# Kernel optimization log

Measured on AMD Instinct MI355X. Metric: run time of the kernel, lower is better.

The kernel has to match this reference:

```python
import jax, jax.numpy as jnp
import numpy as np

K = 64  # key_features
V = 64  # value_features


def setup_inputs() -> dict:
    key = jax.random.key(0)
    ks = jax.random.split(key, 7)
    B, IN, M = 512, 512, 2048
    H = 2 * K + V  # 192, hidden_state dim == output dim of layer
    return {
        "x": jax.random.normal(ks[0], (B, IN), dtype=jnp.float32),
        "hidden_state": jax.random.normal(ks[1], (B, H), dtype=jnp.float32),
        "content": jax.random.normal(ks[2], (B, V), dtype=jnp.float32),
        "key_mem": jax.random.normal(ks[3], (B, K, M), dtype=jnp.float32),
        "value_mem": jax.random.normal(ks[4], (B, V, M), dtype=jnp.float32),
        "W": jax.random.normal(ks[5], (H, IN + 2 * K + 2 * V), dtype=jnp.float32) * 0.02,
        "b": jax.random.normal(ks[6], (H,), dtype=jnp.float32) * 0.02,
    }


def reference(x, hidden_state, content, key_mem, value_mem, W, b):
    # dropout in eval mode (identity); relu on hidden_state
    inp = jnp.concatenate([x, jax.nn.relu(hidden_state), content], axis=1)  # [B, IN+2K+2V]
    o = inp @ W.T + b  # [B, 2K+V]
    query = o[:, :K]            # [B, K]
    # buffer.read: attention over memory slots
    scores = jnp.einsum("bkm,bk->bm", key_mem, query)   # [B, M]
    attn = jax.nn.softmax(scores, axis=1)               # [B, M]
    content_new = jnp.einsum("bvm,bm->bv", value_mem, attn)  # [B, V]
    # buffer.write (state update, returned for completeness of math; original
    # mutates buffer in place; key @ II is exactly a right-shift by one slot):
    new_key = o[:, K:2 * K]
    new_value = o[:, 2 * K:2 * K + V]
    key_mem_next = jnp.concatenate([new_key[:, :, None], key_mem[:, :, :-1]], axis=2)
    value_mem_next = jnp.concatenate([new_value[:, :, None], value_mem[:, :, :-1]], axis=2)
    del key_mem_next, value_mem_next  # forward output matches original: (o, content)
    return (o, content_new)
```

## Files before the change

kernel.cpp:

```cpp
#include <hip/hip_runtime.h>

#define KDIM 64
#define VDIM 64
#define MDIM 2048
#define BDIM 512
#define INDIM 512
#define HDIM 192
#define CIN 768
#define O_SIZE (BDIM*HDIM)

__global__ __launch_bounds__(512, 4)
void memlinear_kernel(const float* __restrict__ x,
                      const float* __restrict__ hidden,
                      const float* __restrict__ content,
                      const float* __restrict__ key_mem,
                      const float* __restrict__ value_mem,
                      const float* __restrict__ W,
                      const float* __restrict__ bias,
                      float* __restrict__ out)
{
    const int b    = blockIdx.x;
    const int tid  = threadIdx.x;
    const int lane = tid & 63;
    const int wid  = tid >> 6;

    __shared__ __align__(16) float inp[CIN];
    __shared__ float q[KDIM];
    __shared__ float red[8];
    __shared__ __align__(16) float attn_lds[MDIM];

    if (tid < INDIM) inp[tid] = x[(size_t)b*INDIM + tid];
    if (tid < HDIM)  inp[INDIM + tid] = fmaxf(hidden[(size_t)b*HDIM + tid], 0.f);
    if (tid < VDIM)  inp[INDIM + HDIM + tid] = content[(size_t)b*VDIM + tid];
    __syncthreads();

    if (tid < HDIM) {
        const float4* w4 = reinterpret_cast<const float4*>(W) + (size_t)tid * (CIN/4);
        const float4* i4 = reinterpret_cast<const float4*>(inp);
        float ax = 0.f, ay = 0.f, az = 0.f, aw = 0.f;
        #pragma unroll 8
        for (int i = 0; i < CIN/4; ++i) {
            float4 w = w4[i];
            float4 v = i4[i];
            ax = fmaf(w.x, v.x, ax);
            ay = fmaf(w.y, v.y, ay);
            az = fmaf(w.z, v.z, az);
            aw = fmaf(w.w, v.w, aw);
        }
        float o = (ax + ay) + (az + aw) + bias[tid];
        out[(size_t)b*HDIM + tid] = o;
        if (tid < KDIM) q[tid] = o;
    }
    __syncthreads();

    const float4* km4 = reinterpret_cast<const float4*>(key_mem + (size_t)b*KDIM*MDIM);
    float4 s = make_float4(0.f, 0.f, 0.f, 0.f);
    #pragma unroll 8
    for (int k = 0; k < KDIM; ++k) {
        float qk = q[k];
        float4 kk = km4[(size_t)k*(MDIM/4) + tid];
        s.x = fmaf(qk, kk.x, s.x);
        s.y = fmaf(qk, kk.y, s.y);
        s.z = fmaf(qk, kk.z, s.z);
        s.w = fmaf(qk, kk.w, s.w);
    }

    float mx = fmaxf(fmaxf(s.x, s.y), fmaxf(s.z, s.w));
    #pragma unroll
    for (int off = 32; off >= 1; off >>= 1)
        mx = fmaxf(mx, __shfl_xor(mx, off));
    if (lane == 0) red[wid] = mx;
    __syncthreads();
    float m_all = red[0];
    #pragma unroll
    for (int w = 1; w < 8; ++w) m_all = fmaxf(m_all, red[w]);

    float4 e;
    e.x = __expf(s.x - m_all);
    e.y = __expf(s.y - m_all);
    e.z = __expf(s.z - m_all);
    e.w = __expf(s.w - m_all);
    float sum = (e.x + e.y) + (e.z + e.w);
    #pragma unroll
    for (int off = 32; off >= 1; off >>= 1)
        sum += __shfl_xor(sum, off);
    __syncthreads();
    if (lane == 0) red[wid] = sum;
    __syncthreads();
    float total = 0.f;
    #pragma unroll
    for (int w = 0; w < 8; ++w) total += red[w];
    float inv = 1.0f / total;

    reinterpret_cast<float4*>(attn_lds)[tid] =
        make_float4(e.x*inv, e.y*inv, e.z*inv, e.w*inv);
    __syncthreads();

    const float4* vm4 = reinterpret_cast<const float4*>(value_mem + (size_t)b*VDIM*MDIM);
    const float4* a4  = reinterpret_cast<const float4*>(attn_lds);
    #pragma unroll
    for (int vi = 0; vi < 8; ++vi) {
        int v = wid*8 + vi;
        float px = 0.f, py = 0.f, pz = 0.f, pw = 0.f;
        #pragma unroll
        for (int i = 0; i < 8; ++i) {
            float4 vv = vm4[(size_t)v*(MDIM/4) + i*64 + lane];
            float4 aa = a4[i*64 + lane];
            px = fmaf(vv.x, aa.x, px);
            py = fmaf(vv.y, aa.y, py);
            pz = fmaf(vv.z, aa.z, pz);
            pw = fmaf(vv.w, aa.w, pw);
        }
        float p = (px + py) + (pz + pw);
        #pragma unroll
        for (int off = 32; off >= 1; off >>= 1)
            p += __shfl_xor(p, off);
        if (lane == 0) out[O_SIZE + (size_t)b*VDIM + v] = p;
    }
}

extern "C" void kernel_launch(void* const* d_in, const int* in_sizes, int n_in,
                              void* d_out, int out_size, void* d_ws, size_t ws_size,
                              hipStream_t stream) {
    const float* x         = (const float*)d_in[0];
    const float* hidden    = (const float*)d_in[1];
    const float* content   = (const float*)d_in[2];
    const float* key_mem   = (const float*)d_in[3];
    const float* value_mem = (const float*)d_in[4];
    const float* W         = (const float*)d_in[5];
    const float* bias      = (const float*)d_in[6];
    float* out = (float*)d_out;

    memlinear_kernel<<<dim3(BDIM), dim3(512), 0, stream>>>(
        x, hidden, content, key_mem, value_mem, W, bias, out);
}
```

Baseline: 129.0 us.

## Split input projection into a separate tiled GEMM kernel before attention

Moves the per-row linear projection out of the attention kernel into a dedicated shared-memory tiled GEMM over 32x32 output tiles. W is then reused across 32 batch rows instead of being re-read by every one of the 512 blocks. The attention kernel no longer keeps most of its threads idle while 192 threads run a long serial dot product. The cost is an extra launch and a dependency on the GEMM kernel finishing before attention can start.

Result: slower. 156.3 us (+21.2%).

```diff
diff --git a/kernel.cpp b/kernel.cpp
--- a/kernel.cpp
+++ b/kernel.cpp
@@ -9,48 +9,77 @@
 #define CIN 768
 #define O_SIZE (BDIM*HDIM)
 
+__global__ __launch_bounds__(256)
+void gemm_kernel(const float* __restrict__ x, const float* __restrict__ hidden,
+                 const float* __restrict__ content, const float* __restrict__ W,
+                 const float* __restrict__ bias, float* __restrict__ out)
+{
+    const int tid  = threadIdx.x;
+    const int bt   = blockIdx.x & 15;
+    const int jt   = blockIdx.x >> 4;
+    const int tx   = tid & 15;
+    const int ty   = tid >> 4;
+    const int lane = tid & 63;
+    const int wid  = tid >> 6;
+
+    __shared__ float As[64][34];
+    __shared__ float Bs[64][34];
+
+    float acc00 = 0.f, acc01 = 0.f, acc10 = 0.f, acc11 = 0.f;
+
+    for (int k0 = 0; k0 < CIN; k0 += 64) {
+        #pragma unroll
+        for (int i = 0; i < 8; ++i) {
+            const int r = i*4 + wid;
+            const int k = lane;
+            const int c = k0 + k;
+            const int bg = bt*32 + r;
+            float av;
+            if (c < INDIM)             av = x[(size_t)bg*INDIM + c];
+            else if (c < INDIM + HDIM) av = fmaxf(hidden[(size_t)bg*HDIM + (c - INDIM)], 0.f);
+            else                       av = content[(size_t)bg*VDIM + (c - INDIM - HDIM)];
+            As[k][r] = av;
+            const int jg = jt*32 + r;
+            Bs[k][r] = W[(size_t)jg*CIN + c];
+        }
+        __syncthreads();
+        #pragma unroll 16
+        for (int k = 0; k < 64; ++k) {
+            const float a0 = As[k][tx*2], a1 = As[k][tx*2+1];
+            const float b0 = Bs[k][ty*2], b1 = Bs[k][ty*2+1];
+            acc00 = fmaf(a0, b0, acc00);
+            acc01 = fmaf(a0, b1, acc01);
+            acc10 = fmaf(a1, b0, acc10);
+            acc11 = fmaf(a1, b1, acc11);
+        }
+        __syncthreads();
+    }
+
+    const int bg = bt*32 + tx*2;
+    const int jg = jt*32 + ty*2;
+    const float bi0 = bias[jg], bi1 = bias[jg+1];
+    out[(size_t)bg*HDIM + jg]           = acc00 + bi0;
+    out[(size_t)bg*HDIM + jg + 1]       = acc01 + bi1;
+    out[(size_t)(bg+1)*HDIM + jg]       = acc10 + bi0;
+    out[(size_t)(bg+1)*HDIM + jg + 1]   = acc11 + bi1;
+}
+
 __global__ __launch_bounds__(512, 4)
-void memlinear_kernel(const float* __restrict__ x,
-                      const float* __restrict__ hidden,
-                      const float* __restrict__ content,
-                      const float* __restrict__ key_mem,
-                      const float* __restrict__ value_mem,
-                      const float* __restrict__ W,
-                      const float* __restrict__ bias,
-                      float* __restrict__ out)
+void attn_kernel(const float* __restrict__ key_mem,
+                 const float* __restrict__ value_mem,
+                 const float* __restrict__ o,
+                 float* __restrict__ out)
 {
     const int b    = blockIdx.x;
     const int tid  = threadIdx.x;
     const int lane = tid & 63;
     const int wid  = tid >> 6;
 
-    __shared__ __align__(16) float inp[CIN];
     __shared__ float q[KDIM];
     __shared__ float red[8];
     __shared__ __align__(16) float attn_lds[MDIM];
 
-    if (tid < INDIM) inp[tid] = x[(size_t)b*INDIM + tid];
-    if (tid < HDIM)  inp[INDIM + tid] = fmaxf(hidden[(size_t)b*HDIM + tid], 0.f);
-    if (tid < VDIM)  inp[INDIM + HDIM + tid] = content[(size_t)b*VDIM + tid];
-    __syncthreads();
-
-    if (tid < HDIM) {
-        const float4* w4 = reinterpret_cast<const float4*>(W) + (size_t)tid * (CIN/4);
-        const float4* i4 = reinterpret_cast<const float4*>(inp);
-        float ax = 0.f, ay = 0.f, az = 0.f, aw = 0.f;
-        #pragma unroll 8
-        for (int i = 0; i < CIN/4; ++i) {
-            float4 w = w4[i];
-            float4 v = i4[i];
-            ax = fmaf(w.x, v.x, ax);
-            ay = fmaf(w.y, v.y, ay);
-            az = fmaf(w.z, v.z, az);
-            aw = fmaf(w.w, v.w, aw);
-        }
-        float o = (ax + ay) + (az + aw) + bias[tid];
-        out[(size_t)b*HDIM + tid] = o;
-        if (tid < KDIM) q[tid] = o;
-    }
+    if (tid < KDIM) q[tid] = o[(size_t)b*HDIM + tid];
     __syncthreads();
 
     const float4* km4 = reinterpret_cast<const float4*>(key_mem + (size_t)b*KDIM*MDIM);
@@ -131,6 +160,6 @@
     const float* bias      = (const float*)d_in[6];
     float* out = (float*)d_out;
 
-    memlinear_kernel<<<dim3(BDIM), dim3(512), 0, stream>>>(
-        x, hidden, content, key_mem, value_mem, W, bias, out);
+    gemm_kernel<<<dim3(96),   dim3(256), 0, stream>>>(x, hidden, content, W, bias, out);
+    attn_kernel<<<dim3(BDIM), dim3(512), 0, stream>>>(key_mem, value_mem, out, out);
 }
```
